# Kernel tuning notes

Hardware: AMD Instinct MI355X
Metric: run time of the kernel (lower is better)

Reference implementation:

```python
import jax, jax.numpy as jnp
import numpy as np

QMIN, QMAX = -128.0, 127.0

def _affine_quantize(x):
    # per-tensor asymmetric int8 activation quantization
    amin, amax = jnp.min(x), jnp.max(x)
    scale = jnp.maximum((amax - amin) / 255.0, 1e-8)
    zp = jnp.clip(jnp.round(-amin / scale) + QMIN, QMIN, QMAX)
    q = jnp.clip(jnp.round(x / scale) + zp, QMIN, QMAX)
    return q, scale, zp

def _sym_quantize(w):
    # per-tensor symmetric int8 weight quantization
    scale = jnp.maximum(jnp.max(jnp.abs(w)) / 127.0, 1e-8)
    q = jnp.clip(jnp.round(w / scale), -127.0, 127.0)
    return q, scale

def _qlinear(x, W, b):
    # quantize input -> integer GEMM (emulated in fp32) -> dequantize
    xq, sx, zx = _affine_quantize(x)
    wq, sw = _sym_quantize(W)
    acc = jnp.einsum('bsh,oh->bso', xq - zx, wq)  # int accumulate, fp32-emulated
    return acc * (sx * sw) + b


def setup_inputs() -> dict:
    key = jax.random.key(0)
    k1, k2, k3, k4, k5 = jax.random.split(key, 5)
    d, h = 1024, 4096
    x = jax.random.normal(k1, (4, 4096, d), dtype=jnp.float32)
    W1 = jax.random.normal(k2, (h, d), dtype=jnp.float32) * (1.0 / np.sqrt(d))
    b1 = jax.random.normal(k3, (h,), dtype=jnp.float32) * 0.02
    W2 = jax.random.normal(k4, (d, h), dtype=jnp.float32) * (1.0 / np.sqrt(h))
    b2 = jax.random.normal(k5, (d,), dtype=jnp.float32) * 0.02
    return {"x": x, "W1": W1, "b1": b1, "W2": W2, "b2": b2}


def reference(x, W1, b1, W2, b2):
    # 1. FP32 -> quantize -> INT8 fc1 -> dequantize -> FP32
    h = _qlinear(x, W1, b1)
    # 2. FP32 GELU (torch nn.GELU default: exact erf form); dropout p=0 is identity
    h = jax.nn.gelu(h, approximate=False)
    # 3. FP32 -> quantize -> INT8 fc2 -> dequantize -> FP32
    out = _qlinear(h, W2, b2)
    return out
```

## Files before the change

### kernel.cpp

```cpp
#include <hip/hip_runtime.h>
#include <hip/hip_bf16.h>
#include <math.h>

#define D_IN   1024
#define D_HID  4096
#define M_TOK  16384

typedef int v4i __attribute__((ext_vector_type(4)));
typedef _Float16 f16x8 __attribute__((ext_vector_type(8)));

typedef __attribute__((address_space(3))) unsigned int lds_u32;
typedef const __attribute__((address_space(1))) unsigned int glb_u32;

__device__ inline void gload_lds16(const signed char* g, signed char* l) {
    __builtin_amdgcn_global_load_lds((glb_u32*)g, (lds_u32*)l, 16, 0, 0);
}

__device__ inline float fast_erf(float x) {
    float ax = fabsf(x);
    float t = __builtin_amdgcn_rcpf(fmaf(0.3275911f, ax, 1.0f));
    float y = t * (0.254829592f +
              t * (-0.284496736f +
              t * (1.421413741f +
              t * (-1.453152027f +
              t * 1.061405429f))));
    float e = __expf(-ax * ax);
    float r = fmaf(-y, e, 1.0f);
    return copysignf(r, x);
}

#define OFF_SLOTS  ((size_t)0)
#define OFF_SCAL   ((size_t)64)
#define OFF_ISCAL  ((size_t)128)
#define OFF_XQ     ((size_t)256)
#define OFF_W1Q    (OFF_XQ  + (size_t)M_TOK * D_IN)
#define OFF_W2Q    (OFF_W1Q + (size_t)D_HID * D_IN)
#define OFF_RS1    (OFF_W2Q + (size_t)D_IN * D_HID)
#define OFF_RS2    (OFF_RS1 + (size_t)D_HID * 4)
#define OFF_H      (OFF_RS2 + (size_t)D_IN * 4 + 128)
#define OFF_HQ     (OFF_H   + (size_t)M_TOK * D_HID * 2)


__device__ inline unsigned enc_f(float f) {
    unsigned u = __float_as_uint(f);
    return (u & 0x80000000u) ? ~u : (u | 0x80000000u);
}
__device__ inline float dec_f(unsigned u) {
    return __uint_as_float((u & 0x80000000u) ? (u ^ 0x80000000u) : ~u);
}

__global__ void k_reduce_all(const float4* __restrict__ x,
                             const float4* __restrict__ w1,
                             const float4* __restrict__ w2,
                             float* __restrict__ pxmin, float* __restrict__ pxmax,
                             float* __restrict__ pw1, float* __restrict__ pw2) {
    __shared__ float red[8];
    const int b = blockIdx.x;
    const int wave = threadIdx.x >> 6, lane = threadIdx.x & 63;
    if (b < 1024) {
        float vmin = 3.4e38f, vmax = -3.4e38f;
        for (int i = b * 256 + threadIdx.x; i < M_TOK * D_IN / 4; i += 1024 * 256) {
            float4 v = x[i];
            vmin = fminf(vmin, fminf(fminf(v.x, v.y), fminf(v.z, v.w)));
            vmax = fmaxf(vmax, fmaxf(fmaxf(v.x, v.y), fmaxf(v.z, v.w)));
        }
        for (int off = 32; off > 0; off >>= 1) {
            vmin = fminf(vmin, __shfl_down(vmin, off));
            vmax = fmaxf(vmax, __shfl_down(vmax, off));
        }
        if (lane == 0) { red[wave] = vmin; red[4 + wave] = vmax; }
        __syncthreads();
        if (threadIdx.x == 0) {
            pxmin[b] = fminf(fminf(red[0], red[1]), fminf(red[2], red[3]));
            pxmax[b] = fmaxf(fmaxf(red[4], red[5]), fmaxf(red[6], red[7]));
        }
    } else {
        const float4* w = (b < 1280) ? w1 : w2;
        const int bb = (b < 1280) ? b - 1024 : b - 1280;
        float vmax = 0.0f;
        for (int i = bb * 256 + threadIdx.x; i < D_HID * D_IN / 4; i += 256 * 256) {
            float4 v = w[i];
            vmax = fmaxf(vmax, fmaxf(fmaxf(fabsf(v.x), fabsf(v.y)), fmaxf(fabsf(v.z), fabsf(v.w))));
        }
        for (int off = 32; off > 0; off >>= 1)
            vmax = fmaxf(vmax, __shfl_down(vmax, off));
        if (lane == 0) red[wave] = vmax;
        __syncthreads();
        if (threadIdx.x == 0) {
            float bm = fmaxf(fmaxf(red[0], red[1]), fmaxf(red[2], red[3]));
            if (b < 1280) pw1[bb] = bm; else pw2[bb] = bm;
        }
    }
}

__global__ void k_scales_all(const float* __restrict__ pxmin, const float* __restrict__ pxmax,
                             const float* __restrict__ pw1, const float* __restrict__ pw2,
                             float* scal, int* iscal, unsigned* slots) {
    const int lane = threadIdx.x;
    float vmin = 3.4e38f, vmax = -3.4e38f;
    for (int i = lane; i < 1024; i += 64) {
        vmin = fminf(vmin, pxmin[i]);
        vmax = fmaxf(vmax, pxmax[i]);
    }
    float w1m = 0.0f, w2m = 0.0f;
    for (int i = lane; i < 256; i += 64) {
        w1m = fmaxf(w1m, pw1[i]);
        w2m = fmaxf(w2m, pw2[i]);
    }
    for (int off = 32; off > 0; off >>= 1) {
        vmin = fminf(vmin, __shfl_down(vmin, off));
        vmax = fmaxf(vmax, __shfl_down(vmax, off));
        w1m  = fmaxf(w1m,  __shfl_down(w1m, off));
        w2m  = fmaxf(w2m,  __shfl_down(w2m, off));
    }
    if (lane == 0) {
        float sx = fmaxf((vmax - vmin) / 255.0f, 1e-8f);
        float zx = rintf(-vmin / sx) - 128.0f;
        zx = fminf(fmaxf(zx, -128.0f), 127.0f);
        float sw1 = fmaxf(w1m / 127.0f, 1e-8f);
        float sw2 = fmaxf(w2m / 127.0f, 1e-8f);
        scal[0] = sx; scal[1] = zx; scal[2] = sw1; scal[3] = sw2; scal[4] = sx * sw1;
        iscal[0] = (int)zx;
        slots[4] = 0xFFFFFFFFu;
        slots[5] = 0u;
    }
}

__global__ void k_quant_all(const float4* __restrict__ x, int* __restrict__ xq,
                            const float* __restrict__ W1, signed char* __restrict__ w1q,
                            int* __restrict__ rs1,
                            const float* __restrict__ W2, signed char* __restrict__ w2q,
                            int* __restrict__ rs2,
                            const float* __restrict__ scal) {
    __shared__ int red[4];
    const int b = blockIdx.x;
    if (b < 2048) {
        float s = scal[0], zp = scal[1];
        for (int i = b * 256 + threadIdx.x; i < M_TOK * D_IN / 4; i += 2048 * 256) {
            float4 v = x[i];
            int a0 = (int)fminf(fmaxf(rintf(v.x / s) + zp, -128.0f), 127.0f);
            int a1 = (int)fminf(fmaxf(rintf(v.y / s) + zp, -128.0f), 127.0f);
            int a2 = (int)fminf(fmaxf(rintf(v.z / s) + zp, -128.0f), 127.0f);
            int a3 = (int)fminf(fmaxf(rintf(v.w / s) + zp, -128.0f), 127.0f);
            xq[i] = (a0 & 255) | ((a1 & 255) << 8) | ((a2 & 255) << 16) | ((a3 & 255) << 24);
        }
        return;
    }
    const int isW1 = (b < 2048 + 4096);
    const int row = isW1 ? (b - 2048) : (b - 6144);
    const int K = isW1 ? D_IN : D_HID;
    const float s = isW1 ? scal[2] : scal[3];
    const float* W = isW1 ? W1 : W2;
    signed char* Wq = isW1 ? w1q : w2q;
    int* rsum = isW1 ? rs1 : rs2;

    const float4* Wr = (const float4*)(W + (size_t)row * K);
    int* out = (int*)(Wq + (size_t)row * K);
    int mysum = 0;
    for (int i = threadIdx.x; i < K / 4; i += 256) {
        float4 v = Wr[i];
        int a0 = (int)fminf(fmaxf(rintf(v.x / s), -127.0f), 127.0f);
        int a1 = (int)fminf(fmaxf(rintf(v.y / s), -127.0f), 127.0f);
        int a2 = (int)fminf(fmaxf(rintf(v.z / s), -127.0f), 127.0f);
        int a3 = (int)fminf(fmaxf(rintf(v.w / s), -127.0f), 127.0f);
        mysum += a0 + a1 + a2 + a3;
        out[i] = (a0 & 255) | ((a1 & 255) << 8) | ((a2 & 255) << 16) | ((a3 & 255) << 24);
    }
    for (int off = 32; off > 0; off >>= 1)
        mysum += __shfl_down(mysum, off);
    const int wave = threadIdx.x >> 6, lane = threadIdx.x & 63;
    if (lane == 0) red[wave] = mysum;
    __syncthreads();
    if (threadIdx.x == 0) rsum[row] = red[0] + red[1] + red[2] + red[3];
}

__global__ void k_quant_h(const f16x8* __restrict__ H, int2* __restrict__ Hq, int n8,
                          const unsigned* __restrict__ slots) {
    float amin = dec_f(slots[4]), amax = dec_f(slots[5]);
    float s = fmaxf((amax - amin) / 255.0f, 1e-8f);
    float zp = rintf(-amin / s) - 128.0f;
    zp = fminf(fmaxf(zp, -128.0f), 127.0f);
    for (int i = blockIdx.x * blockDim.x + threadIdx.x; i < n8; i += gridDim.x * blockDim.x) {
        f16x8 v = H[i];
        int q[8];
#pragma unroll
        for (int j = 0; j < 8; j++)
            q[j] = ((int)fminf(fmaxf(rintf((float)v[j] / s) + zp, -128.0f), 127.0f)) & 255;
        int lo = q[0] | (q[1] << 8) | (q[2] << 16) | (q[3] << 24);
        int hi = q[4] | (q[5] << 8) | (q[6] << 16) | (q[7] << 24);
        Hq[i] = make_int2(lo, hi);
    }
}

__device__ inline void int8_mainloop256(const signed char* __restrict__ A,
                                        const signed char* __restrict__ B,
                                        int K, int m0, int n0,
                                        signed char* Ls, v4i (&acc)[8][4]) {
    const int tid = threadIdx.x;
    const int l = tid & 63, w = tid >> 6;
    const int lm = l & 15, lq = l >> 4;
    const int wmi = w >> 1, wni = w & 1;

    const int gc16 = ((l & 3) ^ ((l >> 3) & 3)) << 4;
    const int srow = (w << 4) + (l >> 2);
    const signed char* gA = A + (long)(m0 + srow) * K + gc16;
    const signed char* gB = B + (long)(n0 + srow) * K + gc16;
    const long rstep = (long)K << 6;
    signed char* lA = Ls + (w << 10) + (l << 4);
    signed char* lB = Ls + 16384 + (w << 10) + (l << 4);

    const int f16off = (lq ^ ((lm >> 1) & 3)) << 4;
    const int aoff = ((wmi << 7) + lm) * 64 + f16off;
    const int boff = 16384 + ((wni << 6) + lm) * 64 + f16off;

    const int KT = K >> 6;

    auto stage = [&](int bufoff, int kt) {
        const signed char* a = gA + ((long)kt << 6);
        const signed char* b = gB + ((long)kt << 6);
        gload_lds16(a,             lA + bufoff);
        gload_lds16(a + rstep,     lA + bufoff + 4096);
        gload_lds16(a + 2 * rstep, lA + bufoff + 8192);
        gload_lds16(a + 3 * rstep, lA + bufoff + 12288);
        gload_lds16(b,             lB + bufoff);
        gload_lds16(b + rstep,     lB + bufoff + 4096);
    };

    auto compute = [&](int bufoff) {
        v4i av[8], bv[4];
#pragma unroll
        for (int j = 0; j < 4; ++j)
            bv[j] = *(const v4i*)&Ls[bufoff + boff + j * 1024];
#pragma unroll
        for (int i = 0; i < 8; ++i)
            av[i] = *(const v4i*)&Ls[bufoff + aoff + i * 1024];
        __builtin_amdgcn_s_setprio(1);
#pragma unroll
        for (int i = 0; i < 8; ++i)
#pragma unroll
            for (int j = 0; j < 4; ++j)
                acc[i][j] = __builtin_amdgcn_mfma_i32_16x16x64_i8(av[i], bv[j], acc[i][j], 0, 0, 0);
        __builtin_amdgcn_s_setprio(0);
    };

    stage(0, 0);
    stage(24576, 1);

    int b0 = 0, b1 = 24576, b2 = 49152;
    for (int t = 0; t < KT - 2; ++t) {
        asm volatile("s_waitcnt vmcnt(6)\n\ts_barrier" ::: "memory");
        stage(b2, t + 2);
        compute(b0);
        int tmp = b0; b0 = b1; b1 = b2; b2 = tmp;
    }
    asm volatile("s_waitcnt vmcnt(6)\n\ts_barrier" ::: "memory");
    compute(b0);
    asm volatile("s_waitcnt vmcnt(0)\n\ts_barrier" ::: "memory");
    compute(b1);
}

__global__ __launch_bounds__(256, 2) void k_gemm1(const signed char* __restrict__ Aq,
                                                  const signed char* __restrict__ Bq,
                                                  _Float16* __restrict__ H,
                                                  const float* __restrict__ scal,
                                                  const int* __restrict__ iscal,
                                                  const int* __restrict__ rsum,
                                                  const float* __restrict__ bias,
                                                  unsigned* slots) {
    __shared__ __align__(16) signed char Ls[3 * 24576];
    __shared__ float red[8];
    const int nb = D_HID / 128;
    const int m0 = (blockIdx.x / nb) * 256, n0 = (blockIdx.x % nb) * 128;
    v4i acc[8][4];
    v4i zero = {0, 0, 0, 0};
#pragma unroll
    for (int i = 0; i < 8; i++)
#pragma unroll
        for (int j = 0; j < 4; j++) acc[i][j] = zero;
    int8_mainloop256(Aq, Bq, D_IN, m0, n0, Ls, acc);

    const int tid = threadIdx.x, l = tid & 63, w = tid >> 6;
    const int lm = l & 15, lq = l >> 4;
    const int wmi = w >> 1, wni = w & 1;
    float s1 = scal[4];
    int zx = iscal[0];
    float lmin = 3.4e38f, lmax = -3.4e38f;

    __syncthreads();

#pragma unroll
    for (int j = 0; j < 4; j++) {
        int n = n0 + (wni << 6) + j * 16 + lm;
        int rsn = rsum[n];
        float bn = bias[n];
        int colb = ((wni << 6) + j * 16 + lm) * 2;
#pragma unroll
        for (int i = 0; i < 8; i++) {
#pragma unroll
            for (int rg = 0; rg < 4; rg++) {
                int row = (wmi << 7) + i * 16 + lq * 4 + rg;
                int v = acc[i][j][rg] - zx * rsn;
                float fv = (float)v * s1 + bn;
                float g = fv * 0.5f * (1.0f + fast_erf(fv * 0.7071067811865476f));
                _Float16 gh = (_Float16)g;
                int off = (row * 256 + colb) ^ (((row >> 2) & 7) << 5);
                *(_Float16*)&Ls[off] = gh;
                float gf = (float)gh;
                lmin = fminf(lmin, gf);
                lmax = fmaxf(lmax, gf);
            }
        }
    }
    __syncthreads();

#pragma unroll
    for (int it = 0; it < 16; it++) {
        int row = it * 16 + (tid >> 4);
        int c = tid & 15;
        int off = (row * 256 + c * 16) ^ (((row >> 2) & 7) << 5);
        v4i d = *(const v4i*)&Ls[off];
        *(v4i*)&H[(long)(m0 + row) * D_HID + n0 + c * 8] = d;
    }

    for (int off = 32; off > 0; off >>= 1) {
        lmin = fminf(lmin, __shfl_down(lmin, off));
        lmax = fmaxf(lmax, __shfl_down(lmax, off));
    }
    if (l == 0) { red[w] = lmin; red[4 + w] = lmax; }
    __syncthreads();
    if (tid == 0) {
        atomicMin(&slots[4], enc_f(fminf(fminf(red[0], red[1]), fminf(red[2], red[3]))));
        atomicMax(&slots[5], enc_f(fmaxf(fmaxf(red[4], red[5]), fmaxf(red[6], red[7]))));
    }
}

__global__ __launch_bounds__(256, 2) void k_gemm2(const signed char* __restrict__ Aq,
                                                  const signed char* __restrict__ Bq,
                                                  float* __restrict__ Out,
                                                  const float* __restrict__ scal,
                                                  const unsigned* __restrict__ slots,
                                                  const int* __restrict__ rsum,
                                                  const float* __restrict__ bias) {
    __shared__ __align__(16) signed char Ls[3 * 24576];
    const int nb = D_IN / 128;
    const int m0 = (blockIdx.x / nb) * 256, n0 = (blockIdx.x % nb) * 128;
    v4i acc[8][4];
    v4i zero = {0, 0, 0, 0};
#pragma unroll
    for (int i = 0; i < 8; i++)
#pragma unroll
        for (int j = 0; j < 4; j++) acc[i][j] = zero;
    int8_mainloop256(Aq, Bq, D_HID, m0, n0, Ls, acc);

    const int tid = threadIdx.x, l = tid & 63, w = tid >> 6;
    const int lm = l & 15, lq = l >> 4;
    const int wmi = w >> 1, wni = w & 1;
    float amin = dec_f(slots[4]), amax = dec_f(slots[5]);
    float sh = fmaxf((amax - amin) / 255.0f, 1e-8f);
    float zpf = rintf(-amin / sh) - 128.0f;
    zpf = fminf(fmaxf(zpf, -128.0f), 127.0f);
    float s2 = sh * scal[3];
    int zx = (int)zpf;
#pragma unroll
    for (int j = 0; j < 4; j++) {
        int n = n0 + (wni << 6) + j * 16 + lm;
        int rsn = rsum[n];
        float bn = bias[n];
#pragma unroll
        for (int i = 0; i < 8; i++) {
            int mb = m0 + (wmi << 7) + i * 16 + lq * 4;
#pragma unroll
            for (int rg = 0; rg < 4; rg++) {
                int v = acc[i][j][rg] - zx * rsn;
                Out[(long)(mb + rg) * D_IN + n] = (float)v * s2 + bn;
            }
        }
    }
}

extern "C" void kernel_launch(void* const* d_in, const int* in_sizes, int n_in,
                              void* d_out, int out_size, void* d_ws, size_t ws_size,
                              hipStream_t stream) {
    const float* x  = (const float*)d_in[0];
    const float* W1 = (const float*)d_in[1];
    const float* b1 = (const float*)d_in[2];
    const float* W2 = (const float*)d_in[3];
    const float* b2 = (const float*)d_in[4];

    char* ws = (char*)d_ws;
    unsigned* slots    = (unsigned*)(ws + OFF_SLOTS);
    float* scal        = (float*)(ws + OFF_SCAL);
    int* iscal         = (int*)(ws + OFF_ISCAL);
    signed char* xq    = (signed char*)(ws + OFF_XQ);
    signed char* w1q   = (signed char*)(ws + OFF_W1Q);
    signed char* w2q   = (signed char*)(ws + OFF_W2Q);
    int* rs1           = (int*)(ws + OFF_RS1);
    int* rs2           = (int*)(ws + OFF_RS2);
    _Float16* h        = (_Float16*)(ws + OFF_H);
    signed char* hq    = (signed char*)(ws + OFF_HQ);

    float* pxmin = (float*)(ws + OFF_RS1);
    float* pxmax = pxmin + 1024;
    float* pw1   = (float*)(ws + OFF_RS2);
    float* pw2   = pw1 + 256;

    k_reduce_all<<<1536, 256, 0, stream>>>((const float4*)x, (const float4*)W1,
                                           (const float4*)W2, pxmin, pxmax, pw1, pw2);
    k_scales_all<<<1, 64, 0, stream>>>(pxmin, pxmax, pw1, pw2, scal, iscal, slots);
    k_quant_all<<<7168, 256, 0, stream>>>((const float4*)x, (int*)xq,
                                          W1, w1q, rs1, W2, w2q, rs2, scal);
    k_gemm1<<<(M_TOK / 256) * (D_HID / 128), 256, 0, stream>>>(xq, w1q, h, scal, iscal, rs1, b1, slots);
    k_quant_h<<<4096, 256, 0, stream>>>((const f16x8*)h, (int2*)hq, M_TOK * D_HID / 8, slots);
    k_gemm2<<<(M_TOK / 256) * (D_IN / 128), 256, 0, stream>>>(hq, w2q, (float*)d_out, scal, slots, rs2, b2);
}
```

Measured before the change: 427.9 us.

## Interleave global-to-LDS loads with MFMA phases in int8 GEMM mainloop

```diff
diff --git a/kernel.cpp b/kernel.cpp
--- a/kernel.cpp
+++ b/kernel.cpp
@@ -192,6 +192,32 @@
     }
 }
 
+#define MFMA_I8(va, vb, c) __builtin_amdgcn_mfma_i32_16x16x64_i8(va, vb, c, 0, 0, 0)
+
+#define PHASE(IP, DMA_STMT, WAIT_STMT)                                           \
+    {                                                                            \
+        v4i a0 = *(const v4i*)&Ls[b0 + aoff + (2 * (IP)) * 1024];                \
+        v4i a1 = *(const v4i*)&Ls[b0 + aoff + (2 * (IP) + 1) * 1024];            \
+        if ((IP) == 0) {                                                         \
+            bv[0] = *(const v4i*)&Ls[b0 + boff + 0 * 1024];                      \
+            bv[1] = *(const v4i*)&Ls[b0 + boff + 1 * 1024];                      \
+            bv[2] = *(const v4i*)&Ls[b0 + boff + 2 * 1024];                      \
+            bv[3] = *(const v4i*)&Ls[b0 + boff + 3 * 1024];                      \
+        }                                                                        \
+        DMA_STMT                                                                 \
+        WAIT_STMT                                                                \
+        asm volatile("s_barrier" ::: "memory");                                  \
+        __builtin_amdgcn_s_setprio(1);                                           \
+        _Pragma("unroll")                                                        \
+        for (int j = 0; j < 4; ++j)                                              \
+            acc[2 * (IP)][j] = MFMA_I8(a0, bv[j], acc[2 * (IP)][j]);             \
+        _Pragma("unroll")                                                        \
+        for (int j = 0; j < 4; ++j)                                              \
+            acc[2 * (IP) + 1][j] = MFMA_I8(a1, bv[j], acc[2 * (IP) + 1][j]);     \
+        __builtin_amdgcn_s_setprio(0);                                           \
+        asm volatile("s_barrier" ::: "memory");                                  \
+    }
+
 __device__ inline void int8_mainloop256(const signed char* __restrict__ A,
                                         const signed char* __restrict__ B,
                                         int K, int m0, int n0,
@@ -215,48 +241,51 @@
 
     const int KT = K >> 6;
 
-    auto stage = [&](int bufoff, int kt) {
-        const signed char* a = gA + ((long)kt << 6);
-        const signed char* b = gB + ((long)kt << 6);
-        gload_lds16(a,             lA + bufoff);
-        gload_lds16(a + rstep,     lA + bufoff + 4096);
-        gload_lds16(a + 2 * rstep, lA + bufoff + 8192);
-        gload_lds16(a + 3 * rstep, lA + bufoff + 12288);
-        gload_lds16(b,             lB + bufoff);
-        gload_lds16(b + rstep,     lB + bufoff + 4096);
-    };
-
-    auto compute = [&](int bufoff) {
-        v4i av[8], bv[4];
-#pragma unroll
-        for (int j = 0; j < 4; ++j)
-            bv[j] = *(const v4i*)&Ls[bufoff + boff + j * 1024];
-#pragma unroll
-        for (int i = 0; i < 8; ++i)
-            av[i] = *(const v4i*)&Ls[bufoff + aoff + i * 1024];
-        __builtin_amdgcn_s_setprio(1);
-#pragma unroll
-        for (int i = 0; i < 8; ++i)
-#pragma unroll
-            for (int j = 0; j < 4; ++j)
-                acc[i][j] = __builtin_amdgcn_mfma_i32_16x16x64_i8(av[i], bv[j], acc[i][j], 0, 0, 0);
-        __builtin_amdgcn_s_setprio(0);
-    };
-
-    stage(0, 0);
-    stage(24576, 1);
+    {
+        const signed char* a = gA;
+        const signed char* b = gB;
+        gload_lds16(a,             lA);
+        gload_lds16(a + rstep,     lA + 4096);
+        gload_lds16(a + 2 * rstep, lA + 8192);
+        gload_lds16(a + 3 * rstep, lA + 12288);
+        gload_lds16(b,             lB);
+        gload_lds16(b + rstep,     lB + 4096);
+        a = gA + 64; b = gB + 64;
+        gload_lds16(a,             lA + 24576);
+        gload_lds16(a + rstep,     lA + 24576 + 4096);
+        gload_lds16(a + 2 * rstep, lA + 24576 + 8192);
+        gload_lds16(a + 3 * rstep, lA + 24576 + 12288);
+        gload_lds16(b,             lB + 24576);
+        gload_lds16(b + rstep,     lB + 24576 + 4096);
+    }
+    asm volatile("s_waitcnt vmcnt(6)\n\ts_barrier" ::: "memory");
 
     int b0 = 0, b1 = 24576, b2 = 49152;
-    for (int t = 0; t < KT - 2; ++t) {
-        asm volatile("s_waitcnt vmcnt(6)\n\ts_barrier" ::: "memory");
-        stage(b2, t + 2);
-        compute(b0);
+    for (int t = 0; t < KT; ++t) {
+        const bool st = (t + 2 < KT);
+        const long go = (long)(t + 2) << 6;
+        v4i bv[4];
+        PHASE(0,
+              if (st) { gload_lds16(gA + go, lA + b2);
+                        gload_lds16(gA + go + rstep, lA + b2 + 4096); },
+              )
+        PHASE(1,
+              if (st) { gload_lds16(gA + go + 2 * rstep, lA + b2 + 8192);
+                        gload_lds16(gA + go + 3 * rstep, lA + b2 + 12288); },
+              )
+        PHASE(2,
+              if (st) { gload_lds16(gB + go, lB + b2);
+                        gload_lds16(gB + go + rstep, lB + b2 + 4096); },
+              )
+        if (st) {
+            PHASE(3, , asm volatile("s_waitcnt vmcnt(6)" ::: "memory");)
+        } else if (t + 1 < KT) {
+            PHASE(3, , asm volatile("s_waitcnt vmcnt(0)" ::: "memory");)
+        } else {
+            PHASE(3, , )
+        }
         int tmp = b0; b0 = b1; b1 = b2; b2 = tmp;
     }
-    asm volatile("s_waitcnt vmcnt(6)\n\ts_barrier" ::: "memory");
-    compute(b0);
-    asm volatile("s_waitcnt vmcnt(0)\n\ts_barrier" ::: "memory");
-    compute(b1);
 }
 
 __global__ __launch_bounds__(256, 2) void k_gemm1(const signed char* __restrict__ Aq,
```

New measurement: 427.6 us. Within noise of the previous version (-0.1%).

## Switch int8 GEMM mainloop to double buffering and raise occupancy to three blocks

Applied to the files above, without the earlier changes.

```diff
diff --git a/kernel.cpp b/kernel.cpp
--- a/kernel.cpp
+++ b/kernel.cpp
@@ -244,22 +244,21 @@
     };
 
     stage(0, 0);
-    stage(24576, 1);
-
-    int b0 = 0, b1 = 24576, b2 = 49152;
-    for (int t = 0; t < KT - 2; ++t) {
-        asm volatile("s_waitcnt vmcnt(6)\n\ts_barrier" ::: "memory");
-        stage(b2, t + 2);
-        compute(b0);
-        int tmp = b0; b0 = b1; b1 = b2; b2 = tmp;
-    }
-    asm volatile("s_waitcnt vmcnt(6)\n\ts_barrier" ::: "memory");
-    compute(b0);
-    asm volatile("s_waitcnt vmcnt(0)\n\ts_barrier" ::: "memory");
-    compute(b1);
-}
-
-__global__ __launch_bounds__(256, 2) void k_gemm1(const signed char* __restrict__ Aq,
+
+    for (int t = 0; t < KT; ++t) {
+        const int cur = (t & 1) * 24576;
+        if (t + 1 < KT) {
+            stage(24576 - cur, t + 1);
+            asm volatile("s_waitcnt vmcnt(6)\n\ts_barrier" ::: "memory");
+        } else {
+            asm volatile("s_waitcnt vmcnt(0)\n\ts_barrier" ::: "memory");
+        }
+        compute(cur);
+        asm volatile("s_barrier" ::: "memory");
+    }
+}
+
+__global__ __launch_bounds__(256, 3) void k_gemm1(const signed char* __restrict__ Aq,
                                                   const signed char* __restrict__ Bq,
                                                   _Float16* __restrict__ H,
                                                   const float* __restrict__ scal,
@@ -267,7 +266,7 @@
                                                   const int* __restrict__ rsum,
                                                   const float* __restrict__ bias,
                                                   unsigned* slots) {
-    __shared__ __align__(16) signed char Ls[3 * 24576];
+    __shared__ __align__(16) signed char Ls[2 * 24576];
     __shared__ float red[8];
     const int nb = D_HID / 128;
     const int m0 = (blockIdx.x / nb) * 256, n0 = (blockIdx.x % nb) * 128;
@@ -285,47 +284,32 @@
     float s1 = scal[4];
     int zx = iscal[0];
     float lmin = 3.4e38f, lmax = -3.4e38f;
-
-    __syncthreads();
-
 #pragma unroll
     for (int j = 0; j < 4; j++) {
         int n = n0 + (wni << 6) + j * 16 + lm;
         int rsn = rsum[n];
         float bn = bias[n];
-        int colb = ((wni << 6) + j * 16 + lm) * 2;
 #pragma unroll
         for (int i = 0; i < 8; i++) {
+            int mb = m0 + (wmi << 7) + i * 16 + lq * 4;
 #pragma unroll
             for (int rg = 0; rg < 4; rg++) {
-                int row = (wmi << 7) + i * 16 + lq * 4 + rg;
                 int v = acc[i][j][rg] - zx * rsn;
                 float fv = (float)v * s1 + bn;
                 float g = fv * 0.5f * (1.0f + fast_erf(fv * 0.7071067811865476f));
                 _Float16 gh = (_Float16)g;
-                int off = (row * 256 + colb) ^ (((row >> 2) & 7) << 5);
-                *(_Float16*)&Ls[off] = gh;
+                H[(long)(mb + rg) * D_HID + n] = gh;
                 float gf = (float)gh;
                 lmin = fminf(lmin, gf);
                 lmax = fmaxf(lmax, gf);
             }
         }
     }
-    __syncthreads();
-
-#pragma unroll
-    for (int it = 0; it < 16; it++) {
-        int row = it * 16 + (tid >> 4);
-        int c = tid & 15;
-        int off = (row * 256 + c * 16) ^ (((row >> 2) & 7) << 5);
-        v4i d = *(const v4i*)&Ls[off];
-        *(v4i*)&H[(long)(m0 + row) * D_HID + n0 + c * 8] = d;
-    }
-
     for (int off = 32; off > 0; off >>= 1) {
         lmin = fminf(lmin, __shfl_down(lmin, off));
         lmax = fmaxf(lmax, __shfl_down(lmax, off));
     }
+    __syncthreads();
     if (l == 0) { red[w] = lmin; red[4 + w] = lmax; }
     __syncthreads();
     if (tid == 0) {
@@ -334,14 +318,14 @@
     }
 }
 
-__global__ __launch_bounds__(256, 2) void k_gemm2(const signed char* __restrict__ Aq,
+__global__ __launch_bounds__(256, 3) void k_gemm2(const signed char* __restrict__ Aq,
                                                   const signed char* __restrict__ Bq,
                                                   float* __restrict__ Out,
                                                   const float* __restrict__ scal,
                                                   const unsigned* __restrict__ slots,
                                                   const int* __restrict__ rsum,
                                                   const float* __restrict__ bias) {
-    __shared__ __align__(16) signed char Ls[3 * 24576];
+    __shared__ __align__(16) signed char Ls[2 * 24576];
     const int nb = D_IN / 128;
     const int m0 = (blockIdx.x / nb) * 256, n0 = (blockIdx.x % nb) * 128;
     v4i acc[8][4];
```

Result: slower. 746.5 us (+74.5%).

## Fold scale computation into quantize kernel and swizzle GEMM blocks across XCDs

Applied to the files above, without the earlier changes.

```diff
diff --git a/kernel.cpp b/kernel.cpp
--- a/kernel.cpp
+++ b/kernel.cpp
@@ -93,49 +93,52 @@
     }
 }
 
-__global__ void k_scales_all(const float* __restrict__ pxmin, const float* __restrict__ pxmax,
-                             const float* __restrict__ pw1, const float* __restrict__ pw2,
-                             float* scal, int* iscal, unsigned* slots) {
-    const int lane = threadIdx.x;
-    float vmin = 3.4e38f, vmax = -3.4e38f;
-    for (int i = lane; i < 1024; i += 64) {
-        vmin = fminf(vmin, pxmin[i]);
-        vmax = fmaxf(vmax, pxmax[i]);
-    }
-    float w1m = 0.0f, w2m = 0.0f;
-    for (int i = lane; i < 256; i += 64) {
-        w1m = fmaxf(w1m, pw1[i]);
-        w2m = fmaxf(w2m, pw2[i]);
-    }
-    for (int off = 32; off > 0; off >>= 1) {
-        vmin = fminf(vmin, __shfl_down(vmin, off));
-        vmax = fmaxf(vmax, __shfl_down(vmax, off));
-        w1m  = fmaxf(w1m,  __shfl_down(w1m, off));
-        w2m  = fmaxf(w2m,  __shfl_down(w2m, off));
-    }
-    if (lane == 0) {
-        float sx = fmaxf((vmax - vmin) / 255.0f, 1e-8f);
-        float zx = rintf(-vmin / sx) - 128.0f;
-        zx = fminf(fmaxf(zx, -128.0f), 127.0f);
-        float sw1 = fmaxf(w1m / 127.0f, 1e-8f);
-        float sw2 = fmaxf(w2m / 127.0f, 1e-8f);
-        scal[0] = sx; scal[1] = zx; scal[2] = sw1; scal[3] = sw2; scal[4] = sx * sw1;
-        iscal[0] = (int)zx;
-        slots[4] = 0xFFFFFFFFu;
-        slots[5] = 0u;
-    }
-}
-
 __global__ void k_quant_all(const float4* __restrict__ x, int* __restrict__ xq,
                             const float* __restrict__ W1, signed char* __restrict__ w1q,
                             int* __restrict__ rs1,
                             const float* __restrict__ W2, signed char* __restrict__ w2q,
                             int* __restrict__ rs2,
-                            const float* __restrict__ scal) {
+                            const float* __restrict__ pxmin, const float* __restrict__ pxmax,
+                            const float* __restrict__ pw1, const float* __restrict__ pw2,
+                            float* __restrict__ scal, int* __restrict__ iscal,
+                            unsigned* __restrict__ slots) {
+    __shared__ float sred[8];
     __shared__ int red[4];
     const int b = blockIdx.x;
+    const int wave = threadIdx.x >> 6, lane = threadIdx.x & 63;
+
     if (b < 2048) {
-        float s = scal[0], zp = scal[1];
+        float vmin = 3.4e38f, vmax = -3.4e38f;
+        for (int i = threadIdx.x; i < 1024; i += 256) {
+            vmin = fminf(vmin, pxmin[i]);
+            vmax = fmaxf(vmax, pxmax[i]);
+        }
+        for (int off = 32; off > 0; off >>= 1) {
+            vmin = fminf(vmin, __shfl_down(vmin, off));
+            vmax = fmaxf(vmax, __shfl_down(vmax, off));
+        }
+        if (lane == 0) { sred[wave] = vmin; sred[4 + wave] = vmax; }
+        __syncthreads();
+        vmin = fminf(fminf(sred[0], sred[1]), fminf(sred[2], sred[3]));
+        vmax = fmaxf(fmaxf(sred[4], sred[5]), fmaxf(sred[6], sred[7]));
+        float s = fmaxf((vmax - vmin) / 255.0f, 1e-8f);
+        float zp = rintf(-vmin / s) - 128.0f;
+        zp = fminf(fmaxf(zp, -128.0f), 127.0f);
+
+        if (b == 0 && threadIdx.x == 0) {
+            float w1m = 0.0f, w2m = 0.0f;
+            for (int i = 0; i < 256; i++) {
+                w1m = fmaxf(w1m, pw1[i]);
+                w2m = fmaxf(w2m, pw2[i]);
+            }
+            float sw1 = fmaxf(w1m / 127.0f, 1e-8f);
+            float sw2 = fmaxf(w2m / 127.0f, 1e-8f);
+            scal[0] = s; scal[1] = zp; scal[2] = sw1; scal[3] = sw2; scal[4] = s * sw1;
+            iscal[0] = (int)zp;
+            slots[4] = 0xFFFFFFFFu;
+            slots[5] = 0u;
+        }
+
         for (int i = b * 256 + threadIdx.x; i < M_TOK * D_IN / 4; i += 2048 * 256) {
             float4 v = x[i];
             int a0 = (int)fminf(fmaxf(rintf(v.x / s) + zp, -128.0f), 127.0f);
@@ -146,13 +149,22 @@
         }
         return;
     }
+
     const int isW1 = (b < 2048 + 4096);
     const int row = isW1 ? (b - 2048) : (b - 6144);
     const int K = isW1 ? D_IN : D_HID;
-    const float s = isW1 ? scal[2] : scal[3];
+    const float* pw = isW1 ? pw1 : pw2;
     const float* W = isW1 ? W1 : W2;
     signed char* Wq = isW1 ? w1q : w2q;
     int* rsum = isW1 ? rs1 : rs2;
+
+    float wm = pw[threadIdx.x & 255];
+    for (int off = 32; off > 0; off >>= 1)
+        wm = fmaxf(wm, __shfl_down(wm, off));
+    if (lane == 0) sred[wave] = wm;
+    __syncthreads();
+    wm = fmaxf(fmaxf(sred[0], sred[1]), fmaxf(sred[2], sred[3]));
+    const float s = fmaxf(wm / 127.0f, 1e-8f);
 
     const float4* Wr = (const float4*)(W + (size_t)row * K);
     int* out = (int*)(Wq + (size_t)row * K);
@@ -168,7 +180,6 @@
     }
     for (int off = 32; off > 0; off >>= 1)
         mysum += __shfl_down(mysum, off);
-    const int wave = threadIdx.x >> 6, lane = threadIdx.x & 63;
     if (lane == 0) red[wave] = mysum;
     __syncthreads();
     if (threadIdx.x == 0) rsum[row] = red[0] + red[1] + red[2] + red[3];
@@ -257,6 +268,11 @@
     compute(b0);
     asm volatile("s_waitcnt vmcnt(0)\n\ts_barrier" ::: "memory");
     compute(b1);
+}
+
+__device__ inline int xcd_swizzle(int b, int nwg) {
+    const int cpx = nwg >> 3;
+    return (b & 7) * cpx + (b >> 3);
 }
 
 __global__ __launch_bounds__(256, 2) void k_gemm1(const signed char* __restrict__ Aq,
@@ -270,7 +286,8 @@
     __shared__ __align__(16) signed char Ls[3 * 24576];
     __shared__ float red[8];
     const int nb = D_HID / 128;
-    const int m0 = (blockIdx.x / nb) * 256, n0 = (blockIdx.x % nb) * 128;
+    const int bid = xcd_swizzle(blockIdx.x, (M_TOK / 256) * nb);
+    const int m0 = (bid / nb) * 256, n0 = (bid % nb) * 128;
     v4i acc[8][4];
     v4i zero = {0, 0, 0, 0};
 #pragma unroll
@@ -343,7 +360,8 @@
                                                   const float* __restrict__ bias) {
     __shared__ __align__(16) signed char Ls[3 * 24576];
     const int nb = D_IN / 128;
-    const int m0 = (blockIdx.x / nb) * 256, n0 = (blockIdx.x % nb) * 128;
+    const int bid = xcd_swizzle(blockIdx.x, (M_TOK / 256) * nb);
+    const int m0 = (bid / nb) * 256, n0 = (bid % nb) * 128;
     v4i acc[8][4];
     v4i zero = {0, 0, 0, 0};
 #pragma unroll
@@ -399,16 +417,16 @@
     _Float16* h        = (_Float16*)(ws + OFF_H);
     signed char* hq    = (signed char*)(ws + OFF_HQ);
 
-    float* pxmin = (float*)(ws + OFF_RS1);
+    float* pxmin = (float*)(ws + OFF_HQ);
     float* pxmax = pxmin + 1024;
-    float* pw1   = (float*)(ws + OFF_RS2);
+    float* pw1   = pxmax + 1024;
     float* pw2   = pw1 + 256;
 
     k_reduce_all<<<1536, 256, 0, stream>>>((const float4*)x, (const float4*)W1,
                                            (const float4*)W2, pxmin, pxmax, pw1, pw2);
-    k_scales_all<<<1, 64, 0, stream>>>(pxmin, pxmax, pw1, pw2, scal, iscal, slots);
     k_quant_all<<<7168, 256, 0, stream>>>((const float4*)x, (int*)xq,
-                                          W1, w1q, rs1, W2, w2q, rs2, scal);
+                                          W1, w1q, rs1, W2, w2q, rs2,
+                                          pxmin, pxmax, pw1, pw2, scal, iscal, slots);
     k_gemm1<<<(M_TOK / 256) * (D_HID / 128), 256, 0, stream>>>(xq, w1q, h, scal, iscal, rs1, b1, slots);
     k_quant_h<<<4096, 256, 0, stream>>>((const f16x8*)h, (int2*)hq, M_TOK * D_HID / 8, slots);
     k_gemm2<<<(M_TOK / 256) * (D_IN / 128), 256, 0, stream>>>(hq, w2q, (float*)d_out, scal, slots, rs2, b2);
```

After: 410.6 us. -4.0%, faster.
